# Performance work log

Measured on AMD Instinct MI355X. Metric: run time of the kernel, lower is better.

The kernel has to match this reference:

```python
import jax, jax.numpy as jnp
import numpy as np

LN_EPS = 1e-5


def _layernorm(x, g, b):
    m = jnp.mean(x, axis=-1, keepdims=True)
    v = jnp.mean((x - m) ** 2, axis=-1, keepdims=True)
    return (x - m) * jax.lax.rsqrt(v + LN_EPS) * g + b


def _gcn_conv(x, row, col, ew, W, b):
    # linear projection
    x = x @ W + b  # [N, out]
    n = x.shape[0]
    # weighted degree per source node (index_add over row)
    deg = jax.ops.segment_sum(ew, row, num_segments=n)  # [N]
    safe = jnp.where(deg > 0, deg, 1.0)
    dis = jnp.where(deg > 0, jax.lax.rsqrt(safe), 0.0)  # deg^-0.5, inf -> 0
    norm = dis[row] * ew * dis[col]  # [E]
    # gather-scale-scatter aggregation
    return jax.ops.segment_sum(norm[:, None] * x[col], row, num_segments=n)


def setup_inputs() -> dict:
    key = jax.random.key(0)
    ks = jax.random.split(key, 8)
    N, E, D_IN, D_H, D_OUT = 50000, 800000, 384, 256, 128
    x = jax.random.normal(ks[0], (N, D_IN), dtype=jnp.float32)
    edge_index = jax.random.randint(ks[1], (2, E), 0, N, dtype=jnp.int64)
    edge_weight = jax.random.uniform(ks[2], (E,), dtype=jnp.float32)
    W1 = jax.random.normal(ks[3], (D_IN, D_H), dtype=jnp.float32) * 0.02
    b1 = jnp.zeros((D_H,), dtype=jnp.float32)
    W2 = jax.random.normal(ks[4], (D_H, D_OUT), dtype=jnp.float32) * 0.02
    b2 = jnp.zeros((D_OUT,), dtype=jnp.float32)
    g1 = jnp.ones((D_H,), dtype=jnp.float32)
    be1 = jnp.zeros((D_H,), dtype=jnp.float32)
    g2 = jnp.ones((D_OUT,), dtype=jnp.float32)
    be2 = jnp.zeros((D_OUT,), dtype=jnp.float32)
    return {"x": x, "edge_index": edge_index, "edge_weight": edge_weight,
            "W1": W1, "b1": b1, "W2": W2, "b2": b2,
            "g1": g1, "be1": be1, "g2": g2, "be2": be2}


def reference(x, edge_index, edge_weight, W1, b1, W2, b2, g1, be1, g2, be2):
    row, col = edge_index[0], edge_index[1]
    h = _gcn_conv(x, row, col, edge_weight, W1, b1)
    h = _layernorm(h, g1, be1)
    h = jax.nn.relu(h)
    # dropout is identity in eval mode
    h = _gcn_conv(h, row, col, edge_weight, W2, b2)
    h = _layernorm(h, g2, be2)
    return h
```

## Files before the change

kernel.cpp:

```cpp
#include <hip/hip_runtime.h>


constexpr float LN_EPS = 1e-5f;

typedef __attribute__((ext_vector_type(8))) short short8;
typedef __attribute__((ext_vector_type(4))) float f32x4;

static __device__ __forceinline__ unsigned short f2bf(float f) {
    unsigned u = __float_as_uint(f);
    u += 0x7FFFu + ((u >> 16) & 1u);
    return (unsigned short)(u >> 16);
}
static __device__ __forceinline__ float bf2f(unsigned short h) {
    return __uint_as_float(((unsigned)h) << 16);
}
static __device__ __forceinline__ short8 f2bf8(float4 a, float4 b) {
    short8 r;
    r[0] = (short)f2bf(a.x); r[1] = (short)f2bf(a.y);
    r[2] = (short)f2bf(a.z); r[3] = (short)f2bf(a.w);
    r[4] = (short)f2bf(b.x); r[5] = (short)f2bf(b.y);
    r[6] = (short)f2bf(b.z); r[7] = (short)f2bf(b.w);
    return r;
}

#if defined(__has_builtin)
#if __has_builtin(__builtin_amdgcn_global_load_lds)
#define HAS_GLL 1
#endif
#endif

#ifdef HAS_GLL
static __device__ __forceinline__ void gll16(const void* g, void* l) {
    __builtin_amdgcn_global_load_lds(
        (__attribute__((address_space(1))) void*)g,
        (__attribute__((address_space(3))) void*)l, 16, 0, 0);
}
#endif

__global__ __launch_bounds__(256) void k_hist(
    const int* __restrict__ row, const float* __restrict__ ew,
    unsigned long long* __restrict__ packed, int* __restrict__ ord, int E)
{
    int e = blockIdx.x * 256 + threadIdx.x;
    if (e >= E) return;
    int r = row[e];
    unsigned fx = __float2uint_rn(ew[e] * 16777216.0f);
    unsigned long long old =
        atomicAdd(packed + r, (1ULL << 32) | (unsigned long long)fx);
    ord[e] = (int)(old >> 32);
}

__global__ __launch_bounds__(256) void k_dis_part(
    const unsigned long long* __restrict__ packed, float* __restrict__ dis,
    int* __restrict__ part, int n)
{
    int i = blockIdx.x * 256 + threadIdx.x;
    int v = 0;
    if (i < n) {
        unsigned long long p = packed[i];
        float d = (float)(unsigned)(p & 0xFFFFFFFFu) * (1.0f / 16777216.0f);
        dis[i] = d > 0.0f ? rsqrtf(d) : 0.0f;
        v = (int)(p >> 32);
    }
    #pragma unroll
    for (int off = 32; off; off >>= 1) v += __shfl_xor(v, off);
    __shared__ int ws[4];
    if ((threadIdx.x & 63) == 0) ws[threadIdx.x >> 6] = v;
    __syncthreads();
    if (threadIdx.x == 0) part[blockIdx.x] = ws[0] + ws[1] + ws[2] + ws[3];
}

__global__ __launch_bounds__(256) void k_scanpart(int* part, int nparts)
{
    int t = threadIdx.x;
    int v = (t < nparts) ? part[t] : 0;
    __shared__ int s[256];
    s[t] = v; __syncthreads();
    for (int off = 1; off < 256; off <<= 1) {
        int u = (t >= off) ? s[t - off] : 0;
        __syncthreads();
        s[t] += u;
        __syncthreads();
    }
    if (t < nparts) part[t] = s[t] - v;
}

__global__ __launch_bounds__(256) void k_rowptr(
    const unsigned long long* __restrict__ packed, const int* __restrict__ part,
    int* __restrict__ rowptr, int n)
{
    int t = threadIdx.x;
    int i = blockIdx.x * 256 + t;
    int v = (i < n) ? (int)(packed[i] >> 32) : 0;
    __shared__ int s[256];
    s[t] = v; __syncthreads();
    for (int off = 1; off < 256; off <<= 1) {
        int u = (t >= off) ? s[t - off] : 0;
        __syncthreads();
        s[t] += u;
        __syncthreads();
    }
    if (i < n) {
        int base = part[blockIdx.x];
        rowptr[i] = base + s[t] - v;
        if (i == n - 1) rowptr[n] = base + s[t];
    }
}

__global__ __launch_bounds__(256) void k_scatter(
    const int* __restrict__ row, const int* __restrict__ col,
    const float* __restrict__ ew, const float* __restrict__ dis,
    const int* __restrict__ rowptr, const int* __restrict__ ord,
    int2* __restrict__ edges, int E)
{
    int e = blockIdx.x * 256 + threadIdx.x;
    if (e >= E) return;
    int r = row[e], c = col[e];
    int p = rowptr[r] + ord[e];
    edges[p] = make_int2(c, __float_as_int(dis[r] * ew[e] * dis[c]));
}

__global__ __launch_bounds__(256) void k_wt(
    const float* __restrict__ W1, const float* __restrict__ W2,
    unsigned short* __restrict__ W1T, unsigned short* __restrict__ W2T)
{
    constexpr int K1 = 384, N1 = 256, K2 = 256, N2 = 128;
    int o = blockIdx.x * 256 + threadIdx.x;
    if (o < K1 * N1) {
        int n = o / K1, k = o - n * K1;
        W1T[o] = f2bf(W1[(size_t)k * N1 + n]);
    } else {
        int o2 = o - K1 * N1;
        if (o2 < K2 * N2) {
            int n = o2 / K2, k = o2 - n * K2;
            W2T[o2] = f2bf(W2[(size_t)k * N2 + n]);
        }
    }
}

template<bool AF32, int BN>
__global__ __launch_bounds__(256) void k_gemm_mfma(
    const void* __restrict__ Av, const unsigned short* __restrict__ BT,
    const float* __restrict__ bias, unsigned short* __restrict__ C,
    int M, int K)
{
    constexpr int BM = 64, BK = 32;
    constexpr int NF = BN / 64;
    constexpr int AB = (AF32 ? 4 : 2) * BM * BK;
    constexpr int BB = 2 * BN * BK;
    constexpr int ASL = AB / 16;
    constexpr int BSL = BB / 16;
    constexpr int ACH = AF32 ? 8 : 4;

    __shared__ char smem[2 * (AB + BB)];

    const int t    = threadIdx.x;
    const int lane = t & 63;
    const int wid  = t >> 6;
    const int row0 = blockIdx.x * BM;
    const int fr   = lane & 15;
    const int fq   = lane >> 4;
    const int nb   = wid * (BN / 4);

    const float*          Af = (const float*)Av;
    const unsigned short* Ab = (const unsigned short*)Av;

    const int nt = K / BK;
    f32x4 acc[4][NF] = {};

    auto srcA = [&](int s, int k0) -> const void* {
        int r = s / ACH, ch = s - r * ACH;
        int gr = row0 + r; if (gr >= M) gr = M - 1;
        if constexpr (AF32) return (const void*)(Af + (size_t)gr * K + k0 + ch * 4);
        else                return (const void*)(Ab + (size_t)gr * K + k0 + ch * 8);
    };
    auto srcB = [&](int s, int k0) -> const void* {
        int r = s >> 2, ch = s & 3;
        return (const void*)(BT + (size_t)r * K + k0 + ch * 8);
    };

    auto compute = [&](char* As, char* Bs) {
        short8 af[4], bfr[NF];
        #pragma unroll
        for (int i = 0; i < 4; ++i) {
            const int r = i * 16 + fr;
            if constexpr (AF32) {
                const float* p = (const float*)As + r * BK + fq * 8;
                float4 u0 = *(const float4*)p;
                float4 u1 = *(const float4*)(p + 4);
                af[i] = f2bf8(u0, u1);
            } else {
                af[i] = *(const short8*)((const unsigned short*)As + r * BK + fq * 8);
            }
        }
        #pragma unroll
        for (int j = 0; j < NF; ++j)
            bfr[j] = *(const short8*)((const unsigned short*)Bs
                                      + (nb + j * 16 + fr) * BK + fq * 8);
        #pragma unroll
        for (int i = 0; i < 4; ++i)
            #pragma unroll
            for (int j = 0; j < NF; ++j)
                acc[i][j] = __builtin_amdgcn_mfma_f32_16x16x32_bf16(
                    af[i], bfr[j], acc[i][j], 0, 0, 0);
    };

#ifdef HAS_GLL
    auto stage = [&](int buf, int k0) {
        char* As = smem + buf * (AB + BB);
        char* Bs = As + AB;
        #pragma unroll
        for (int c = 0; c < ASL / 256; ++c) {
            const int s = c * 256 + t;
            gll16(srcA(s, k0), As + s * 16);
        }
        #pragma unroll
        for (int c = 0; c < BSL / 256; ++c) {
            const int s = c * 256 + t;
            gll16(srcB(s, k0), Bs + s * 16);
        }
    };

    stage(0, 0);
    __syncthreads();
    int cur = 0;
    for (int st = 0; st < nt; ++st) {
        if (st + 1 < nt) stage(cur ^ 1, (st + 1) * BK);
        char* As = smem + cur * (AB + BB);
        compute(As, As + AB);
        __syncthreads();
        cur ^= 1;
    }
#else
    char* As = smem;
    char* Bs = smem + AB;
    for (int st = 0; st < nt; ++st) {
        const int k0 = st * BK;
        int4 ar[ASL / 256], br[BSL / 256];
        #pragma unroll
        for (int c = 0; c < ASL / 256; ++c)
            ar[c] = *(const int4*)srcA(c * 256 + t, k0);
        #pragma unroll
        for (int c = 0; c < BSL / 256; ++c)
            br[c] = *(const int4*)srcB(c * 256 + t, k0);
        __syncthreads();
        #pragma unroll
        for (int c = 0; c < ASL / 256; ++c)
            *(int4*)(As + (c * 256 + t) * 16) = ar[c];
        #pragma unroll
        for (int c = 0; c < BSL / 256; ++c)
            *(int4*)(Bs + (c * 256 + t) * 16) = br[c];
        __syncthreads();
        compute(As, Bs);
    }
#endif

    #pragma unroll
    for (int i = 0; i < 4; ++i) {
        #pragma unroll
        for (int j = 0; j < NF; ++j) {
            const int c = nb + j * 16 + fr;
            const float bvv = bias[c];
            #pragma unroll
            for (int r = 0; r < 4; ++r) {
                const int rr = row0 + i * 16 + fq * 4 + r;
                if (rr < M)
                    C[(size_t)rr * BN + c] = f2bf(acc[i][j][r] + bvv);
            }
        }
    }
}

template<int D, bool RELU, bool OUTBF>
__global__ __launch_bounds__(256) void k_agg_ln(
    const unsigned short* __restrict__ feat, const int* __restrict__ rowptr,
    const int2* __restrict__ edges,
    const float* __restrict__ g, const float* __restrict__ b,
    void* __restrict__ outv, int n)
{
    constexpr int LPR = D / 8;
    constexpr int EPI = 64 / LPR;
    const int gw   = (blockIdx.x * 256 + threadIdx.x) >> 6;
    const int lane = threadIdx.x & 63;
    if (gw >= n) return;

    const int sub = lane / LPR;
    const int el  = (lane % LPR) * 8;

    float acc[8] = {};
    const int j0 = rowptr[gw], j1 = rowptr[gw + 1];
    #pragma unroll 2
    for (int j = j0; j < j1; j += EPI) {
        const int jj = j + sub;
        float wv = 0.0f;
        int   c  = 0;
        if (jj < j1) {
            int2 e = edges[jj];
            c  = e.x;
            wv = __int_as_float(e.y);
        }
        const short8 u = *(const short8*)(feat + (size_t)c * D + el);
        #pragma unroll
        for (int i = 0; i < 8; ++i)
            acc[i] += wv * bf2f((unsigned short)u[i]);
    }

    #pragma unroll
    for (int off = LPR; off < 64; off <<= 1)
        #pragma unroll
        for (int i = 0; i < 8; ++i)
            acc[i] += __shfl_xor(acc[i], off);

    float s = 0.0f;
    #pragma unroll
    for (int i = 0; i < 8; ++i) s += acc[i];
    #pragma unroll
    for (int off = 32; off; off >>= 1) s += __shfl_xor(s, off);
    const float m = s * (1.0f / (EPI * D));

    float q = 0.0f;
    #pragma unroll
    for (int i = 0; i < 8; ++i) { float d = acc[i] - m; q += d * d; }
    #pragma unroll
    for (int off = 32; off; off >>= 1) q += __shfl_xor(q, off);
    const float r = rsqrtf(q * (1.0f / (EPI * D)) + LN_EPS);

    if (lane < LPR) {
        float4 g0 = *(const float4*)(g + el);
        float4 g1 = *(const float4*)(g + el + 4);
        float4 b0 = *(const float4*)(b + el);
        float4 b1 = *(const float4*)(b + el + 4);
        float gg[8] = {g0.x, g0.y, g0.z, g0.w, g1.x, g1.y, g1.z, g1.w};
        float bb[8] = {b0.x, b0.y, b0.z, b0.w, b1.x, b1.y, b1.z, b1.w};
        float o[8];
        #pragma unroll
        for (int i = 0; i < 8; ++i) {
            float tv = (acc[i] - m) * r * gg[i] + bb[i];
            if constexpr (RELU) tv = fmaxf(tv, 0.0f);
            o[i] = tv;
        }
        if constexpr (OUTBF) {
            short8 u;
            #pragma unroll
            for (int i = 0; i < 8; ++i) u[i] = (short)f2bf(o[i]);
            *(short8*)((unsigned short*)outv + (size_t)gw * D + el) = u;
        } else {
            float* op = (float*)outv + (size_t)gw * D + el;
            *(float4*)(op)     = make_float4(o[0], o[1], o[2], o[3]);
            *(float4*)(op + 4) = make_float4(o[4], o[5], o[6], o[7]);
        }
    }
}

extern "C" void kernel_launch(void* const* d_in, const int* in_sizes, int n_in,
                              void* d_out, int out_size, void* d_ws, size_t ws_size,
                              hipStream_t stream)
{
    (void)n_in; (void)out_size; (void)ws_size;

    constexpr int DIN = 384, DH = 256, DOUT = 128;

    const float* x   = (const float*)d_in[0];
    const int*   ei  = (const int*)  d_in[1];
    const float* ew  = (const float*)d_in[2];
    const float* W1  = (const float*)d_in[3];
    const float* b1  = (const float*)d_in[4];
    const float* W2  = (const float*)d_in[5];
    const float* b2  = (const float*)d_in[6];
    const float* g1  = (const float*)d_in[7];
    const float* be1 = (const float*)d_in[8];
    const float* g2  = (const float*)d_in[9];
    const float* be2 = (const float*)d_in[10];
    float* out = (float*)d_out;

    const int N = in_sizes[0] / DIN;
    const int E = in_sizes[2];
    const int* row = ei;
    const int* col = ei + E;

    char* w = (char*)d_ws;
    auto carve = [&](size_t bytes) {
        char* p = w;
        w += (bytes + 255) & ~(size_t)255;
        return p;
    };
    unsigned long long* packed = (unsigned long long*)carve((size_t)N * 8);
    float*          dis    = (float*)carve((size_t)N * 4);
    int*            rowptr = (int*)  carve((size_t)(N + 1) * 4);
    int*            part   = (int*)  carve(256 * 4);
    int2*           edges  = (int2*) carve((size_t)E * 8);
    unsigned short* W1T    = (unsigned short*)carve((size_t)DIN * DH * 2);
    unsigned short* W2T    = (unsigned short*)carve((size_t)DH * DOUT * 2);
    unsigned short* h1     = (unsigned short*)carve((size_t)N * DH * 2);
    unsigned short* h1ln   = (unsigned short*)carve((size_t)N * DH * 2);
    unsigned short* h2     = (unsigned short*)carve((size_t)N * DOUT * 2);
    int*            ord    = (int*)h1;

    const int gE = (E + 255) / 256;
    const int gN = (N + 255) / 256;
    const int gW = (N + 3) / 4;
    const int gG = (N + 63) / 64;

    hipMemsetAsync(packed, 0, (size_t)N * 8, stream);
    k_hist    <<<gE, 256, 0, stream>>>(row, ew, packed, ord, E);
    k_dis_part<<<gN, 256, 0, stream>>>(packed, dis, part, N);
    k_scanpart<<<1, 256, 0, stream>>>(part, gN);
    k_rowptr  <<<gN, 256, 0, stream>>>(packed, part, rowptr, N);
    k_scatter <<<gE, 256, 0, stream>>>(row, col, ew, dis, rowptr, ord, edges, E);

    k_wt<<<(DIN * DH + DH * DOUT + 255) / 256, 256, 0, stream>>>(W1, W2, W1T, W2T);

    k_gemm_mfma<true, DH><<<gG, 256, 0, stream>>>(x, W1T, b1, h1, N, DIN);
    k_agg_ln<DH, true, true><<<gW, 256, 0, stream>>>(h1, rowptr, edges,
                                                     g1, be1, h1ln, N);

    k_gemm_mfma<false, DOUT><<<gG, 256, 0, stream>>>(h1ln, W2T, b2, h2, N, DH);
    k_agg_ln<DOUT, false, false><<<gW, 256, 0, stream>>>(h2, rowptr, edges,
                                                         g2, be2, out, N);
}
```

Measured before the change: 225.9 us.

## Drop LDS staging in MFMA GEMM and load fragments directly from global

The GEMM kernel no longer stages A and B tiles through double-buffered shared memory with global_load_lds. Each wave now reads its MFMA fragments straight from global memory into registers. K becomes a template parameter so the k-loop unrolls fully, and launch bounds request 4 blocks per CU. This removes LDS traffic and barriers, at the cost of redundant global/L2 reads of B across waves and of A across column waves, plus more register pressure from the full unroll.

```diff
diff --git a/kernel.cpp b/kernel.cpp
--- a/kernel.cpp
+++ b/kernel.cpp
@@ -22,20 +22,6 @@
     r[6] = (short)f2bf(b.z); r[7] = (short)f2bf(b.w);
     return r;
 }
-
-#if defined(__has_builtin)
-#if __has_builtin(__builtin_amdgcn_global_load_lds)
-#define HAS_GLL 1
-#endif
-#endif
-
-#ifdef HAS_GLL
-static __device__ __forceinline__ void gll16(const void* g, void* l) {
-    __builtin_amdgcn_global_load_lds(
-        (__attribute__((address_space(1))) void*)g,
-        (__attribute__((address_space(3))) void*)l, 16, 0, 0);
-}
-#endif
 
 __global__ __launch_bounds__(256) void k_hist(
     const int* __restrict__ row, const float* __restrict__ ew,
@@ -138,21 +124,14 @@
     }
 }
 
-template<bool AF32, int BN>
-__global__ __launch_bounds__(256) void k_gemm_mfma(
+template<bool AF32, int BN, int K>
+__global__ __launch_bounds__(256, 4) void k_gemm_mfma(
     const void* __restrict__ Av, const unsigned short* __restrict__ BT,
-    const float* __restrict__ bias, unsigned short* __restrict__ C,
-    int M, int K)
-{
-    constexpr int BM = 64, BK = 32;
+    const float* __restrict__ bias, unsigned short* __restrict__ C, int M)
+{
+    constexpr int BM = 64;
+    constexpr int BK = 32;
     constexpr int NF = BN / 64;
-    constexpr int AB = (AF32 ? 4 : 2) * BM * BK;
-    constexpr int BB = 2 * BN * BK;
-    constexpr int ASL = AB / 16;
-    constexpr int BSL = BB / 16;
-    constexpr int ACH = AF32 ? 8 : 4;
-
-    __shared__ char smem[2 * (AB + BB)];
 
     const int t    = threadIdx.x;
     const int lane = t & 63;
@@ -165,95 +144,38 @@
     const float*          Af = (const float*)Av;
     const unsigned short* Ab = (const unsigned short*)Av;
 
-    const int nt = K / BK;
+    int arow[4];
+    #pragma unroll
+    for (int i = 0; i < 4; ++i) {
+        int r = row0 + i * 16 + fr;
+        arow[i] = r < M ? r : M - 1;
+    }
+
     f32x4 acc[4][NF] = {};
 
-    auto srcA = [&](int s, int k0) -> const void* {
-        int r = s / ACH, ch = s - r * ACH;
-        int gr = row0 + r; if (gr >= M) gr = M - 1;
-        if constexpr (AF32) return (const void*)(Af + (size_t)gr * K + k0 + ch * 4);
-        else                return (const void*)(Ab + (size_t)gr * K + k0 + ch * 8);
-    };
-    auto srcB = [&](int s, int k0) -> const void* {
-        int r = s >> 2, ch = s & 3;
-        return (const void*)(BT + (size_t)r * K + k0 + ch * 8);
-    };
-
-    auto compute = [&](char* As, char* Bs) {
+    #pragma unroll
+    for (int k0 = 0; k0 < K; k0 += BK) {
         short8 af[4], bfr[NF];
         #pragma unroll
         for (int i = 0; i < 4; ++i) {
-            const int r = i * 16 + fr;
             if constexpr (AF32) {
-                const float* p = (const float*)As + r * BK + fq * 8;
-                float4 u0 = *(const float4*)p;
-                float4 u1 = *(const float4*)(p + 4);
-                af[i] = f2bf8(u0, u1);
+                const float* p = Af + (size_t)arow[i] * K + k0 + fq * 8;
+                af[i] = f2bf8(*(const float4*)p, *(const float4*)(p + 4));
             } else {
-                af[i] = *(const short8*)((const unsigned short*)As + r * BK + fq * 8);
+                af[i] = *(const short8*)(Ab + (size_t)arow[i] * K + k0 + fq * 8);
             }
         }
         #pragma unroll
         for (int j = 0; j < NF; ++j)
-            bfr[j] = *(const short8*)((const unsigned short*)Bs
-                                      + (nb + j * 16 + fr) * BK + fq * 8);
+            bfr[j] = *(const short8*)(BT + (size_t)(nb + j * 16 + fr) * K
+                                      + k0 + fq * 8);
         #pragma unroll
         for (int i = 0; i < 4; ++i)
             #pragma unroll
             for (int j = 0; j < NF; ++j)
                 acc[i][j] = __builtin_amdgcn_mfma_f32_16x16x32_bf16(
                     af[i], bfr[j], acc[i][j], 0, 0, 0);
-    };
-
-#ifdef HAS_GLL
-    auto stage = [&](int buf, int k0) {
-        char* As = smem + buf * (AB + BB);
-        char* Bs = As + AB;
-        #pragma unroll
-        for (int c = 0; c < ASL / 256; ++c) {
-            const int s = c * 256 + t;
-            gll16(srcA(s, k0), As + s * 16);
-        }
-        #pragma unroll
-        for (int c = 0; c < BSL / 256; ++c) {
-            const int s = c * 256 + t;
-            gll16(srcB(s, k0), Bs + s * 16);
-        }
-    };
-
-    stage(0, 0);
-    __syncthreads();
-    int cur = 0;
-    for (int st = 0; st < nt; ++st) {
-        if (st + 1 < nt) stage(cur ^ 1, (st + 1) * BK);
-        char* As = smem + cur * (AB + BB);
-        compute(As, As + AB);
-        __syncthreads();
-        cur ^= 1;
-    }
-#else
-    char* As = smem;
-    char* Bs = smem + AB;
-    for (int st = 0; st < nt; ++st) {
-        const int k0 = st * BK;
-        int4 ar[ASL / 256], br[BSL / 256];
-        #pragma unroll
-        for (int c = 0; c < ASL / 256; ++c)
-            ar[c] = *(const int4*)srcA(c * 256 + t, k0);
-        #pragma unroll
-        for (int c = 0; c < BSL / 256; ++c)
-            br[c] = *(const int4*)srcB(c * 256 + t, k0);
-        __syncthreads();
-        #pragma unroll
-        for (int c = 0; c < ASL / 256; ++c)
-            *(int4*)(As + (c * 256 + t) * 16) = ar[c];
-        #pragma unroll
-        for (int c = 0; c < BSL / 256; ++c)
-            *(int4*)(Bs + (c * 256 + t) * 16) = br[c];
-        __syncthreads();
-        compute(As, Bs);
-    }
-#endif
+    }
 
     #pragma unroll
     for (int i = 0; i < 4; ++i) {
@@ -410,11 +332,11 @@
 
     k_wt<<<(DIN * DH + DH * DOUT + 255) / 256, 256, 0, stream>>>(W1, W2, W1T, W2T);
 
-    k_gemm_mfma<true, DH><<<gG, 256, 0, stream>>>(x, W1T, b1, h1, N, DIN);
+    k_gemm_mfma<true, DH, DIN><<<gG, 256, 0, stream>>>(x, W1T, b1, h1, N);
     k_agg_ln<DH, true, true><<<gW, 256, 0, stream>>>(h1, rowptr, edges,
                                                      g1, be1, h1ln, N);
 
-    k_gemm_mfma<false, DOUT><<<gG, 256, 0, stream>>>(h1ln, W2T, b2, h2, N, DH);
+    k_gemm_mfma<false, DOUT, DH><<<gG, 256, 0, stream>>>(h1ln, W2T, b2, h2, N);
     k_agg_ln<DOUT, false, false><<<gW, 256, 0, stream>>>(h2, rowptr, edges,
                                                          g2, be2, out, N);
 }
```

New measurement: 272.1 us. 1.2x slower.
